# Optimization experiments

Measured on AMD Instinct MI355X. Metric: run time of the kernel, lower is better.

The kernel has to match this reference:

```python
import jax, jax.numpy as jnp
import numpy as np

# Dimensions (see init_kwargs): C=out_channels, R=res, PS=pool_size, HN=head_num,
# D=head_dim=R*R//HN, input spatial H=W=PS*R.
B, C, R, PS, HN, D = 16, 512, 32, 3, 8, 128
NORM_C = 0.5


def _avg_pool(x, k):
    b, c, h, w = x.shape
    return x.reshape(b, c, h // k, k, w // k, k).mean(axis=(3, 5))


def _max_pool(x, k):
    b, c, h, w = x.shape
    return x.reshape(b, c, h // k, k, w // k, k).max(axis=(3, 5))


def _to_heads(p):
    # Replicates torch: [B,C,R,R].view(B,R*R,C).permute(0,2,1).view(B,C,HN,D).permute(0,2,1,3)
    t = p.reshape(B, R * R, C).transpose(0, 2, 1)  # [B, C, R*R]
    return t.reshape(B, C, HN, D).transpose(0, 2, 1, 3)  # [B, HN, C, D]


def setup_inputs() -> dict:
    key = jax.random.key(0)
    ks = jax.random.split(key, 6)
    H = PS * R
    x = jax.random.normal(ks[0], (B, C, H, H), jnp.float32)
    # per-head q/k projections (Linear(head_dim, head_dim) per head)
    Wqk = jax.random.normal(ks[1], (HN, D, D), jnp.float32) * (1.0 / np.sqrt(D))
    bqk = jax.random.normal(ks[2], (HN, D), jnp.float32) * 0.01
    # w_p: Linear(C, C) feeding sigmoid gate
    Wp = jax.random.normal(ks[3], (C, C), jnp.float32) * (1.0 / np.sqrt(C))
    bp = jnp.zeros((C,), jnp.float32)
    # w_v: 1x1 Conv2d(C, C)
    Wv = jax.random.normal(ks[4], (C, C), jnp.float32) * (1.0 / np.sqrt(C))
    bv = jax.random.normal(ks[5], (C,), jnp.float32) * 0.01
    return {"x": x, "Wqk": Wqk, "bqk": bqk, "Wp": Wp, "bp": bp,
            "Wv": Wv, "bv": bv, "weight": 0}


def reference(x, Wqk, bqk, Wp, bp, Wv, bv, weight):
    # pooled query / key token grids: [B, C, R, R]
    q_pool = _avg_pool(x, PS)
    k_pool = _max_pool(x, PS)

    # heads over channels: [B, HN, C, D], then per-head linear (torch Linear: y = x W^T + b)
    q = jnp.einsum('bhcd,hed->bhce', _to_heads(q_pool), Wqk) + bqk[None, :, None, :]
    k = jnp.einsum('bhcd,hed->bhce', _to_heads(k_pool), Wqk) + bqk[None, :, None, :]

    # value: 1x1 conv then AvgPool2d(3) -> [B, HN, C, D]
    v_conv = jnp.einsum('bchw,oc->bohw', x, Wv) + bv[None, :, None, None]
    v = _to_heads(_avg_pool(v_conv, 3))

    # channel attention scores: [B, HN, C, C]
    scores = jnp.einsum('bhcd,bhed->bhce', q, k)
    # learned power-law exponent gate: sigmoid(Linear(mean over keys))
    p = jax.nn.sigmoid(scores.mean(axis=-1) @ Wp.T + bp)  # [B, HN, C]
    norm_scores = scores / jnp.power(jnp.float32(D), NORM_C + p[..., None])
    w = jax.nn.softmax(norm_scores, axis=-1)
    attn = jnp.einsum('bhce,bhed->bhcd', w, v)  # [B, HN, C, D]

    # back to [B, R, R, C] (torch permute/view chain)
    attn = attn.transpose(0, 2, 1, 3).reshape(B, C, R * R)
    attn = attn.transpose(0, 2, 1).reshape(B, R, R, C)

    # residual on pooled input (original code's residual shape is inconsistent;
    # we use the pooled token grid, same reshape path as the output)
    resid = q_pool.reshape(B, R * R, C).reshape(B, R, R, C)
    return resid + attn * (1 + weight)
```

## Files before the change

### kernel.cpp

```cpp
#include <hip/hip_runtime.h>
#include <math.h>

typedef unsigned short u16;
typedef short bf16x8 __attribute__((ext_vector_type(8)));
typedef float floatx4 __attribute__((ext_vector_type(4)));

#define F_QP   0ull
#define F_KP   8388608ull
#define F_KBAR 16777216ull
#define F_MROW 16793600ull
#define F_IPW  16859136ull
#define F_RS   16924672ull
#define F_END  16990208ull
#define U_QPT_V 0ull
#define U_QPT_P 8388608ull
#define U_KPT_P 16777216ull
#define U_PQ    25165824ull
#define U_PK    33554432ull
#define U_VP    41943040ull
#define U_E     50331648ull
#define U_WV    83886080ull
#define U_WQK   84148224ull

__device__ __forceinline__ u16 f2bf(float f) {
    union { float f; unsigned u; } v; v.f = f;
    return (u16)((v.u + 0x7fffu + ((v.u >> 16) & 1u)) >> 16);
}
__device__ __forceinline__ float bf2f(u16 u) {
    union { unsigned u; float f; } v; v.u = ((unsigned)u) << 16;
    return v.f;
}
__device__ __forceinline__ void ld_async16(const u16* g, u16* l) {
    __builtin_amdgcn_global_load_lds(
        (const __attribute__((address_space(1))) void*)g,
        (__attribute__((address_space(3))) void*)l, 16, 0, 0);
}

__global__ __launch_bounds__(256) void pool_kernel(const float* __restrict__ x,
                                                   float* __restrict__ qp,
                                                   float* __restrict__ kp) {
    int idx = blockIdx.x * 256 + threadIdx.x;
    int r = idx & 1023;
    int c = (idx >> 10) & 511;
    int b = idx >> 19;
    int i = r >> 5, j = r & 31;
    const float* p = x + b * 4718592 + c * 9216 + (3 * i) * 96 + 3 * j;
    float s = 0.f, mx = -INFINITY;
    #pragma unroll
    for (int di = 0; di < 3; ++di)
        #pragma unroll
        for (int dj = 0; dj < 3; ++dj) {
            float v = p[di * 96 + dj];
            s += v; mx = fmaxf(mx, v);
        }
    qp[idx] = s * (1.f / 9.f);
    kp[idx] = mx;
}

__global__ __launch_bounds__(256) void transpose_cvt(const float* __restrict__ in,
                                                     u16* __restrict__ out,
                                                     int inRows, int inCols) {
    __shared__ float tile[32][33];
    const float* src = in + (size_t)blockIdx.z * 524288;
    u16* dst = out + (size_t)blockIdx.z * 524288;
    int c0 = blockIdx.x * 32, r0 = blockIdx.y * 32;
    int tx = threadIdx.x & 31, ty = threadIdx.x >> 5;
    #pragma unroll
    for (int it = 0; it < 4; ++it)
        tile[ty + it * 8][tx] = src[(size_t)(r0 + ty + it * 8) * inCols + c0 + tx];
    __syncthreads();
    #pragma unroll
    for (int it = 0; it < 4; ++it)
        dst[(size_t)(c0 + ty + it * 8) * inRows + r0 + tx] = f2bf(tile[tx][ty + it * 8]);
}

__global__ __launch_bounds__(256) void cvt_bf16(const float* __restrict__ in,
                                                u16* __restrict__ out, int n) {
    int i = blockIdx.x * 256 + threadIdx.x;
    if (i < n) out[i] = f2bf(in[i]);
}

__global__ __launch_bounds__(256) void zero_f32(float* __restrict__ p, int n) {
    int i = blockIdx.x * 256 + threadIdx.x;
    if (i < n) p[i] = 0.f;
}

__device__ __forceinline__ void gemm_bt_body(const u16* __restrict__ A, int ldA,
                                             const u16* __restrict__ B, int ldB, int K,
                                             u16* As, u16* Bs, floatx4 (&acc)[4][4]) {
    const int tid = threadIdx.x;
    const int lane = tid & 63;
    const int wv = tid >> 6;
    const int wm = (wv & 1) * 64, wn = (wv >> 1) * 64;
    const u16* ga0 = A + (size_t)(tid >> 2) * ldA + (tid & 3) * 8;
    const u16* ga1 = A + (size_t)((tid >> 2) + 64) * ldA + (tid & 3) * 8;
    const u16* gb0 = B + (size_t)(tid >> 2) * ldB + (tid & 3) * 8;
    const u16* gb1 = B + (size_t)((tid >> 2) + 64) * ldB + (tid & 3) * 8;
    u16* la0 = As + tid * 8;
    u16* la1 = As + (tid + 256) * 8;
    u16* lb0 = Bs + tid * 8;
    u16* lb1 = Bs + (tid + 256) * 8;
    const int arow = (lane & 15) * 32 + (lane >> 4) * 8;
    for (int k0 = 0; k0 < K; k0 += 32) {
        ld_async16(ga0 + k0, la0);
        ld_async16(ga1 + k0, la1);
        ld_async16(gb0 + k0, lb0);
        ld_async16(gb1 + k0, lb1);
        __syncthreads();
        bf16x8 af[4], bfr[4];
        #pragma unroll
        for (int i = 0; i < 4; ++i)
            af[i] = *(const bf16x8*)&As[(wm + i * 16) * 32 + arow];
        #pragma unroll
        for (int j = 0; j < 4; ++j)
            bfr[j] = *(const bf16x8*)&Bs[(wn + j * 16) * 32 + arow];
        #pragma unroll
        for (int i = 0; i < 4; ++i)
            #pragma unroll
            for (int j = 0; j < 4; ++j)
                acc[i][j] = __builtin_amdgcn_mfma_f32_16x16x32_bf16(af[i], bfr[j], acc[i][j], 0, 0, 0);
        __syncthreads();
    }
}

__global__ __launch_bounds__(256) void vpool_mfma(const u16* __restrict__ Wv_bf,
                                                  const float* __restrict__ bv,
                                                  const u16* __restrict__ qpT_v,
                                                  u16* __restrict__ vp_bf) {
    __shared__ __align__(16) u16 As[4096], Bs[4096];
    floatx4 acc[4][4] = {};
    const int m0 = blockIdx.y * 128, n0 = blockIdx.x * 128, b = blockIdx.z;
    gemm_bt_body(Wv_bf + (size_t)m0 * 512, 512,
                 qpT_v + (size_t)b * 524288 + (size_t)n0 * 512, 512, 512, As, Bs, acc);
    const int tid = threadIdx.x, lane = tid & 63, wv = tid >> 6;
    const int wm = (wv & 1) * 64, wn = (wv >> 1) * 64, col = lane & 15, quad = lane >> 4;
    u16* outb = vp_bf + (size_t)b * 524288;
    #pragma unroll
    for (int i = 0; i < 4; ++i)
        #pragma unroll
        for (int r = 0; r < 4; ++r) {
            int m = m0 + wm + i * 16 + quad * 4 + r;
            float bias = bv[m];
            #pragma unroll
            for (int j = 0; j < 4; ++j) {
                int n = n0 + wn + j * 16 + col;
                outb[(size_t)m * 1024 + n] = f2bf(acc[i][j][r] + bias);
            }
        }
}

__global__ __launch_bounds__(256) void proj_mfma(const u16* __restrict__ qpT_p,
                                                 const u16* __restrict__ kpT_p,
                                                 const u16* __restrict__ Wqk_bf,
                                                 const float* __restrict__ bqk,
                                                 u16* __restrict__ pq_bf,
                                                 u16* __restrict__ pk_bf) {
    __shared__ __align__(16) u16 As[4096], Bs[4096];
    floatx4 acc[4][4] = {};
    const int z = blockIdx.y;
    const int b = z >> 4, h = (z >> 1) & 7, src = z & 1;
    const int m0 = blockIdx.x * 128;
    const u16* P = (src ? kpT_p : qpT_p) + (size_t)b * 524288 + (size_t)m0 * 1024 + h * 128;
    gemm_bt_body(P, 1024, Wqk_bf + h * 16384, 128, 128, As, Bs, acc);
    const int tid = threadIdx.x, lane = tid & 63, wv = tid >> 6;
    const int wm = (wv & 1) * 64, wn = (wv >> 1) * 64, col = lane & 15, quad = lane >> 4;
    u16* outp = (src ? pk_bf : pq_bf) + (size_t)(b * 8 + h) * 65536 + (size_t)m0 * 128;
    #pragma unroll
    for (int i = 0; i < 4; ++i)
        #pragma unroll
        for (int r = 0; r < 4; ++r) {
            int m = wm + i * 16 + quad * 4 + r;
            #pragma unroll
            for (int j = 0; j < 4; ++j) {
                int n = wn + j * 16 + col;
                outp[(size_t)m * 128 + n] = f2bf(acc[i][j][r] + bqk[h * 128 + n]);
            }
        }
}

__global__ __launch_bounds__(128) void kbar_kernel(const u16* __restrict__ pk_bf,
                                                   float* __restrict__ kbar) {
    int bh = blockIdx.x, d = threadIdx.x;
    const u16* p = pk_bf + (size_t)bh * 65536 + d;
    float s = 0.f;
    for (int e = 0; e < 512; ++e) s += bf2f(p[e * 128]);
    kbar[bh * 128 + d] = s * (1.f / 512.f);
}

__global__ __launch_bounds__(256) void mrow_kernel(const u16* __restrict__ pq_bf,
                                                   const float* __restrict__ kbar,
                                                   float* __restrict__ mrow) {
    __shared__ float kb[128];
    int bh = blockIdx.x, tid = threadIdx.x;
    if (tid < 128) kb[tid] = kbar[bh * 128 + tid];
    __syncthreads();
    for (int c = tid; c < 512; c += 256) {
        const u16* q = pq_bf + (size_t)bh * 65536 + c * 128;
        float s = 0.f;
        #pragma unroll 8
        for (int d = 0; d < 128; ++d) s += bf2f(q[d]) * kb[d];
        mrow[bh * 512 + c] = s;
    }
}

__global__ __launch_bounds__(256) void gate_kernel(const float* __restrict__ mrow,
                                                   const float* __restrict__ Wp,
                                                   const float* __restrict__ bp,
                                                   float* __restrict__ ipw) {
    __shared__ float ms[512];
    int bh = blockIdx.x, tid = threadIdx.x;
    for (int c = tid; c < 512; c += 256) ms[c] = mrow[bh * 512 + c];
    __syncthreads();
    for (int c2 = tid; c2 < 512; c2 += 256) {
        const float* wr = Wp + c2 * 512;
        float a = bp[c2];
        #pragma unroll 8
        for (int c = 0; c < 512; ++c) a += ms[c] * wr[c];
        float pg = 1.f / (1.f + expf(-a));
        ipw[bh * 512 + c2] = exp2f(-7.f * (0.5f + pg));
    }
}

__global__ __launch_bounds__(256) void scores_mfma(const u16* __restrict__ pq_bf,
                                                   const u16* __restrict__ pk_bf,
                                                   const float* __restrict__ ipw,
                                                   u16* __restrict__ e_bf,
                                                   float* __restrict__ rowsum) {
    __shared__ __align__(16) u16 As[4096], Bs[4096];
    floatx4 acc[4][4] = {};
    const int n0 = blockIdx.x * 128, m0 = blockIdx.y * 128, bh = blockIdx.z;
    gemm_bt_body(pq_bf + (size_t)bh * 65536 + (size_t)m0 * 128, 128,
                 pk_bf + (size_t)bh * 65536 + (size_t)n0 * 128, 128, 128, As, Bs, acc);
    const int tid = threadIdx.x, lane = tid & 63, wv = tid >> 6;
    const int wm = (wv & 1) * 64, wn = (wv >> 1) * 64, col = lane & 15, quad = lane >> 4;
    u16* ebase = e_bf + (size_t)bh * 262144;
    float* rs = rowsum + bh * 512;
    #pragma unroll
    for (int i = 0; i < 4; ++i)
        #pragma unroll
        for (int r = 0; r < 4; ++r) {
            int m = m0 + wm + i * 16 + quad * 4 + r;
            float sc = ipw[(size_t)bh * 512 + m];
            float p = 0.f;
            #pragma unroll
            for (int j = 0; j < 4; ++j) {
                int n = n0 + wn + j * 16 + col;
                u16 eb = f2bf(expf(acc[i][j][r] * sc));
                ebase[(size_t)m * 512 + n] = eb;
                p += bf2f(eb);
            }
            #pragma unroll
            for (int o = 8; o; o >>= 1) p += __shfl_xor(p, o);
            if (col == 0) atomicAdd(&rs[m], p);
        }
}

__global__ __launch_bounds__(256) void attn_out_mfma(const u16* __restrict__ vp_bf,
                                                     const u16* __restrict__ e_bf,
                                                     const float* __restrict__ rowsum,
                                                     const float* __restrict__ qp,
                                                     float* __restrict__ outp,
                                                     const int* __restrict__ wgt) {
    __shared__ __align__(16) u16 As[4096], Bs[4096];
    floatx4 acc[4][4] = {};
    const int n0 = blockIdx.x * 128, bh = blockIdx.y;
    const int b = bh >> 3, h = bh & 7;
    gemm_bt_body(vp_bf + (size_t)b * 524288 + (size_t)h * 65536, 512,
                 e_bf + (size_t)bh * 262144 + (size_t)n0 * 512, 512, 512, As, Bs, acc);
    const int tid = threadIdx.x, lane = tid & 63, wv = tid >> 6;
    const int wm = (wv & 1) * 64, wn = (wv >> 1) * 64, col = lane & 15, quad = lane >> 4;
    const float mult = 1.f + (float)wgt[0];
    #pragma unroll
    for (int j = 0; j < 4; ++j) {
        int n = n0 + wn + j * 16 + col;
        float inv = mult / rowsum[bh * 512 + n];
        #pragma unroll
        for (int i = 0; i < 4; ++i)
            #pragma unroll
            for (int r = 0; r < 4; ++r) {
                int m = wm + i * 16 + quad * 4 + r;
                size_t o = (size_t)b * 524288 + (size_t)(h * 128 + m) * 512 + n;
                outp[o] = qp[o] + acc[i][j][r] * inv;
            }
    }
}

extern "C" void kernel_launch(void* const* d_in, const int* in_sizes, int n_in,
                              void* d_out, int out_size, void* d_ws, size_t ws_size,
                              hipStream_t stream) {
    const float* x   = (const float*)d_in[0];
    const float* Wqk = (const float*)d_in[1];
    const float* bqk = (const float*)d_in[2];
    const float* Wp  = (const float*)d_in[3];
    const float* bp  = (const float*)d_in[4];
    const float* Wv  = (const float*)d_in[5];
    const float* bv  = (const float*)d_in[6];
    const int*   wgt = (const int*)d_in[7];
    float* out = (float*)d_out;

    float* ws = (float*)d_ws;
    float* qp   = ws + F_QP;
    float* kp   = ws + F_KP;
    float* kbar = ws + F_KBAR;
    float* mrow = ws + F_MROW;
    float* ipw  = ws + F_IPW;
    float* rs   = ws + F_RS;
    u16* ub = (u16*)(ws + F_END);
    u16* qpT_v  = ub + U_QPT_V;
    u16* qpT_p  = ub + U_QPT_P;
    u16* kpT_p  = ub + U_KPT_P;
    u16* pq_bf  = ub + U_PQ;
    u16* pk_bf  = ub + U_PK;
    u16* vp_bf  = ub + U_VP;
    u16* e_bf   = ub + U_E;
    u16* Wv_bf  = ub + U_WV;
    u16* Wqk_bf = ub + U_WQK;

    pool_kernel<<<32768, 256, 0, stream>>>(x, qp, kp);
    transpose_cvt<<<dim3(32, 16, 16), 256, 0, stream>>>(qp, qpT_v, 512, 1024);
    transpose_cvt<<<dim3(16, 32, 16), 256, 0, stream>>>(qp, qpT_p, 1024, 512);
    transpose_cvt<<<dim3(16, 32, 16), 256, 0, stream>>>(kp, kpT_p, 1024, 512);
    cvt_bf16<<<1024, 256, 0, stream>>>(Wv, Wv_bf, 262144);
    cvt_bf16<<<512, 256, 0, stream>>>(Wqk, Wqk_bf, 131072);
    zero_f32<<<256, 256, 0, stream>>>(rs, 65536);

    vpool_mfma<<<dim3(8, 4, 16), 256, 0, stream>>>(Wv_bf, bv, qpT_v, vp_bf);
    proj_mfma<<<dim3(4, 256), 256, 0, stream>>>(qpT_p, kpT_p, Wqk_bf, bqk, pq_bf, pk_bf);
    kbar_kernel<<<128, 128, 0, stream>>>(pk_bf, kbar);
    mrow_kernel<<<128, 256, 0, stream>>>(pq_bf, kbar, mrow);
    gate_kernel<<<128, 256, 0, stream>>>(mrow, Wp, bp, ipw);
    scores_mfma<<<dim3(4, 4, 128), 256, 0, stream>>>(pq_bf, pk_bf, ipw, e_bf, rs);
    attn_out_mfma<<<dim3(4, 128), 256, 0, stream>>>(vp_bf, e_bf, rs, qp, out, wgt);
}
```

Measured before the change: 632.9 us.

## Fuse pooling with transposes, fuse gate kernels, and flash-fuse scores with attention output

Pooling now writes the bf16 transposed layouts directly from a shared-memory tile, replacing three separate transpose passes and the kp buffer. The weight conversions are merged into one kernel, and Wp is pre-transposed so the gate GEMV reads it coalesced. The kbar, mrow and gate kernels become a single kernel. The scores and attention-output GEMMs are fused into one flash-style kernel that keeps the exp tile in LDS, which removes the 32M-element bf16 exp-score buffer and the global atomics for row sums. In exchange the fused kernel launches only 512 blocks, which may hurt occupancy and parallelism, and it uses fast exp without max subtraction.

Result: faster. 596.8 us (-5.7%).

```diff
diff --git a/kernel.cpp b/kernel.cpp
--- a/kernel.cpp
+++ b/kernel.cpp
@@ -6,21 +6,17 @@
 typedef float floatx4 __attribute__((ext_vector_type(4)));
 
 #define F_QP   0ull
-#define F_KP   8388608ull
-#define F_KBAR 16777216ull
-#define F_MROW 16793600ull
-#define F_IPW  16859136ull
-#define F_RS   16924672ull
-#define F_END  16990208ull
+#define F_IPW  8388608ull
+#define F_WPT  8454144ull
+#define F_END  8716288ull
 #define U_QPT_V 0ull
 #define U_QPT_P 8388608ull
 #define U_KPT_P 16777216ull
 #define U_PQ    25165824ull
 #define U_PK    33554432ull
 #define U_VP    41943040ull
-#define U_E     50331648ull
-#define U_WV    83886080ull
-#define U_WQK   84148224ull
+#define U_WV    50331648ull
+#define U_WQK   50593792ull
 
 __device__ __forceinline__ u16 f2bf(float f) {
     union { float f; unsigned u; } v; v.f = f;
@@ -36,53 +32,71 @@
         (__attribute__((address_space(3))) void*)l, 16, 0, 0);
 }
 
-__global__ __launch_bounds__(256) void pool_kernel(const float* __restrict__ x,
-                                                   float* __restrict__ qp,
-                                                   float* __restrict__ kp) {
-    int idx = blockIdx.x * 256 + threadIdx.x;
-    int r = idx & 1023;
-    int c = (idx >> 10) & 511;
-    int b = idx >> 19;
-    int i = r >> 5, j = r & 31;
-    const float* p = x + b * 4718592 + c * 9216 + (3 * i) * 96 + 3 * j;
-    float s = 0.f, mx = -INFINITY;
-    #pragma unroll
-    for (int di = 0; di < 3; ++di)
-        #pragma unroll
-        for (int dj = 0; dj < 3; ++dj) {
-            float v = p[di * 96 + dj];
-            s += v; mx = fmaxf(mx, v);
-        }
-    qp[idx] = s * (1.f / 9.f);
-    kp[idx] = mx;
-}
-
-__global__ __launch_bounds__(256) void transpose_cvt(const float* __restrict__ in,
-                                                     u16* __restrict__ out,
-                                                     int inRows, int inCols) {
-    __shared__ float tile[32][33];
-    const float* src = in + (size_t)blockIdx.z * 524288;
-    u16* dst = out + (size_t)blockIdx.z * 524288;
-    int c0 = blockIdx.x * 32, r0 = blockIdx.y * 32;
+__global__ __launch_bounds__(256) void pool_fused(const float* __restrict__ x,
+                                                  float* __restrict__ qp,
+                                                  u16* __restrict__ qpT_v,
+                                                  u16* __restrict__ qpT_p,
+                                                  u16* __restrict__ kpT_p) {
+    __shared__ float Tq[32][33], Tk[32][33];
+    const int tid = threadIdx.x;
+    const int i  = blockIdx.x;
+    const int c0 = blockIdx.y * 32;
+    const int b  = blockIdx.z;
+    const int j  = tid & 31, cg = tid >> 5;
+    #pragma unroll
+    for (int p = 0; p < 4; ++p) {
+        int cl = p * 8 + cg;
+        const float* px = x + (size_t)b * 4718592 + (size_t)(c0 + cl) * 9216 + (3 * i) * 96 + 3 * j;
+        float s = 0.f, mx = -INFINITY;
+        #pragma unroll
+        for (int di = 0; di < 3; ++di)
+            #pragma unroll
+            for (int dj = 0; dj < 3; ++dj) {
+                float v = px[di * 96 + dj];
+                s += v; mx = fmaxf(mx, v);
+            }
+        float q = s * (1.f / 9.f);
+        Tq[cl][j] = q; Tk[cl][j] = mx;
+        qp[(size_t)b * 524288 + (size_t)(c0 + cl) * 1024 + i * 32 + j] = q;
+    }
+    __syncthreads();
+    const int cl = tid & 31, jq = tid >> 5;
+    const int rh = i >> 4;
+    const int s2 = (c0 + cl) * 2 + rh;
+    #pragma unroll
+    for (int jj = 0; jj < 4; ++jj) {
+        int jw = jq + jj * 8;
+        int rr = i * 32 + jw;
+        int cc = rr & 511;
+        u16 qb = f2bf(Tq[cl][jw]);
+        u16 kb = f2bf(Tk[cl][jw]);
+        qpT_v[(size_t)b * 524288 + (size_t)rr * 512 + c0 + cl] = qb;
+        qpT_p[(size_t)b * 524288 + (size_t)cc * 1024 + s2] = qb;
+        kpT_p[(size_t)b * 524288 + (size_t)cc * 1024 + s2] = kb;
+    }
+}
+
+__global__ __launch_bounds__(256) void cvt_w(const float* __restrict__ Wv,
+                                             const float* __restrict__ Wqk,
+                                             u16* __restrict__ Wv_bf,
+                                             u16* __restrict__ Wqk_bf) {
+    int i = blockIdx.x * 256 + threadIdx.x;
+    if (i < 262144) Wv_bf[i] = f2bf(Wv[i]);
+    else if (i < 393216) Wqk_bf[i - 262144] = f2bf(Wqk[i - 262144]);
+}
+
+__global__ __launch_bounds__(256) void transpose_wp(const float* __restrict__ in,
+                                                    float* __restrict__ out) {
+    __shared__ float t[32][33];
+    int x0 = blockIdx.x * 32, y0 = blockIdx.y * 32;
     int tx = threadIdx.x & 31, ty = threadIdx.x >> 5;
     #pragma unroll
     for (int it = 0; it < 4; ++it)
-        tile[ty + it * 8][tx] = src[(size_t)(r0 + ty + it * 8) * inCols + c0 + tx];
+        t[ty + it * 8][tx] = in[(size_t)(y0 + ty + it * 8) * 512 + x0 + tx];
     __syncthreads();
     #pragma unroll
     for (int it = 0; it < 4; ++it)
-        dst[(size_t)(c0 + ty + it * 8) * inRows + r0 + tx] = f2bf(tile[tx][ty + it * 8]);
-}
-
-__global__ __launch_bounds__(256) void cvt_bf16(const float* __restrict__ in,
-                                                u16* __restrict__ out, int n) {
-    int i = blockIdx.x * 256 + threadIdx.x;
-    if (i < n) out[i] = f2bf(in[i]);
-}
-
-__global__ __launch_bounds__(256) void zero_f32(float* __restrict__ p, int n) {
-    int i = blockIdx.x * 256 + threadIdx.x;
-    if (i < n) p[i] = 0.f;
+        out[(size_t)(x0 + ty + it * 8) * 512 + y0 + tx] = t[tx][ty + it * 8];
 }
 
 __device__ __forceinline__ void gemm_bt_body(const u16* __restrict__ A, int ldA,
@@ -178,109 +192,139 @@
         }
 }
 
-__global__ __launch_bounds__(128) void kbar_kernel(const u16* __restrict__ pk_bf,
-                                                   float* __restrict__ kbar) {
-    int bh = blockIdx.x, d = threadIdx.x;
-    const u16* p = pk_bf + (size_t)bh * 65536 + d;
-    float s = 0.f;
-    for (int e = 0; e < 512; ++e) s += bf2f(p[e * 128]);
-    kbar[bh * 128 + d] = s * (1.f / 512.f);
-}
-
-__global__ __launch_bounds__(256) void mrow_kernel(const u16* __restrict__ pq_bf,
-                                                   const float* __restrict__ kbar,
-                                                   float* __restrict__ mrow) {
+__global__ __launch_bounds__(256) void gate_fused(const u16* __restrict__ pq_bf,
+                                                  const u16* __restrict__ pk_bf,
+                                                  const float* __restrict__ WpT,
+                                                  const float* __restrict__ bp,
+                                                  float* __restrict__ ipw) {
+    __shared__ float sp[256];
     __shared__ float kb[128];
-    int bh = blockIdx.x, tid = threadIdx.x;
-    if (tid < 128) kb[tid] = kbar[bh * 128 + tid];
-    __syncthreads();
-    for (int c = tid; c < 512; c += 256) {
-        const u16* q = pq_bf + (size_t)bh * 65536 + c * 128;
+    __shared__ float ms[512];
+    const int bh = blockIdx.x, tid = threadIdx.x;
+    const u16* pkb = pk_bf + (size_t)bh * 65536;
+    const u16* pqb = pq_bf + (size_t)bh * 65536;
+    {
+        int d = tid & 127, half = tid >> 7;
+        const u16* p = pkb + (size_t)(half * 256) * 128 + d;
+        float s = 0.f;
+        #pragma unroll 8
+        for (int e = 0; e < 256; ++e) s += bf2f(p[(size_t)e * 128]);
+        sp[tid] = s;
+    }
+    __syncthreads();
+    if (tid < 128) kb[tid] = (sp[tid] + sp[tid + 128]) * (1.f / 512.f);
+    __syncthreads();
+    for (int cc = tid; cc < 512; cc += 256) {
+        const u16* q = pqb + (size_t)cc * 128;
         float s = 0.f;
         #pragma unroll 8
         for (int d = 0; d < 128; ++d) s += bf2f(q[d]) * kb[d];
-        mrow[bh * 512 + c] = s;
-    }
-}
-
-__global__ __launch_bounds__(256) void gate_kernel(const float* __restrict__ mrow,
-                                                   const float* __restrict__ Wp,
-                                                   const float* __restrict__ bp,
-                                                   float* __restrict__ ipw) {
-    __shared__ float ms[512];
-    int bh = blockIdx.x, tid = threadIdx.x;
-    for (int c = tid; c < 512; c += 256) ms[c] = mrow[bh * 512 + c];
+        ms[cc] = s;
+    }
     __syncthreads();
     for (int c2 = tid; c2 < 512; c2 += 256) {
-        const float* wr = Wp + c2 * 512;
         float a = bp[c2];
-        #pragma unroll 8
-        for (int c = 0; c < 512; ++c) a += ms[c] * wr[c];
-        float pg = 1.f / (1.f + expf(-a));
+        #pragma unroll 4
+        for (int c = 0; c < 512; ++c) a += ms[c] * WpT[(size_t)c * 512 + c2];
+        float pg = 1.f / (1.f + __expf(-a));
         ipw[bh * 512 + c2] = exp2f(-7.f * (0.5f + pg));
     }
 }
 
-__global__ __launch_bounds__(256) void scores_mfma(const u16* __restrict__ pq_bf,
-                                                   const u16* __restrict__ pk_bf,
-                                                   const float* __restrict__ ipw,
-                                                   u16* __restrict__ e_bf,
-                                                   float* __restrict__ rowsum) {
-    __shared__ __align__(16) u16 As[4096], Bs[4096];
-    floatx4 acc[4][4] = {};
-    const int n0 = blockIdx.x * 128, m0 = blockIdx.y * 128, bh = blockIdx.z;
-    gemm_bt_body(pq_bf + (size_t)bh * 65536 + (size_t)m0 * 128, 128,
-                 pk_bf + (size_t)bh * 65536 + (size_t)n0 * 128, 128, 128, As, Bs, acc);
-    const int tid = threadIdx.x, lane = tid & 63, wv = tid >> 6;
-    const int wm = (wv & 1) * 64, wn = (wv >> 1) * 64, col = lane & 15, quad = lane >> 4;
-    u16* ebase = e_bf + (size_t)bh * 262144;
-    float* rs = rowsum + bh * 512;
-    #pragma unroll
-    for (int i = 0; i < 4; ++i)
-        #pragma unroll
-        for (int r = 0; r < 4; ++r) {
-            int m = m0 + wm + i * 16 + quad * 4 + r;
-            float sc = ipw[(size_t)bh * 512 + m];
-            float p = 0.f;
-            #pragma unroll
-            for (int j = 0; j < 4; ++j) {
-                int n = n0 + wn + j * 16 + col;
-                u16 eb = f2bf(expf(acc[i][j][r] * sc));
-                ebase[(size_t)m * 512 + n] = eb;
-                p += bf2f(eb);
-            }
-            #pragma unroll
-            for (int o = 8; o; o >>= 1) p += __shfl_xor(p, o);
-            if (col == 0) atomicAdd(&rs[m], p);
-        }
-}
-
-__global__ __launch_bounds__(256) void attn_out_mfma(const u16* __restrict__ vp_bf,
-                                                     const u16* __restrict__ e_bf,
-                                                     const float* __restrict__ rowsum,
+__global__ __launch_bounds__(256, 2) void flash_mfma(const u16* __restrict__ pq_bf,
+                                                     const u16* __restrict__ pk_bf,
+                                                     const u16* __restrict__ vp_bf,
+                                                     const float* __restrict__ ipw,
                                                      const float* __restrict__ qp,
                                                      float* __restrict__ outp,
                                                      const int* __restrict__ wgt) {
-    __shared__ __align__(16) u16 As[4096], Bs[4096];
-    floatx4 acc[4][4] = {};
-    const int n0 = blockIdx.x * 128, bh = blockIdx.y;
-    const int b = bh >> 3, h = bh & 7;
-    gemm_bt_body(vp_bf + (size_t)b * 524288 + (size_t)h * 65536, 512,
-                 e_bf + (size_t)bh * 262144 + (size_t)n0 * 512, 512, 512, As, Bs, acc);
+    __shared__ __align__(16) u16 As[4096];
+    __shared__ __align__(16) u16 Bs[4096];
+    __shared__ __align__(16) u16 Et[128 * 136];
+    __shared__ float rsS[128];
+    __shared__ float ipwS[128];
     const int tid = threadIdx.x, lane = tid & 63, wv = tid >> 6;
     const int wm = (wv & 1) * 64, wn = (wv >> 1) * 64, col = lane & 15, quad = lane >> 4;
+    const int bh = blockIdx.y, b = bh >> 3, h = bh & 7;
+    const int m0 = blockIdx.x * 128;
+    if (tid < 128) { rsS[tid] = 0.f; ipwS[tid] = ipw[bh * 512 + m0 + tid]; }
+    const u16* Aq = pq_bf + (size_t)bh * 65536 + (size_t)m0 * 128;
+    const u16* Bk = pk_bf + (size_t)bh * 65536;
+    const u16* Av = vp_bf + (size_t)b * 524288 + (size_t)h * 65536;
+    const int srow = tid >> 2, scol = (tid & 3) * 8;
+    u16 *la0 = As + tid * 8, *la1 = As + (tid + 256) * 8;
+    u16 *lb0 = Bs + tid * 8, *lb1 = Bs + (tid + 256) * 8;
+    const int arow = col * 32 + quad * 8;
+    floatx4 accP[4][4] = {};
+    __syncthreads();
+
+    for (int n0 = 0; n0 < 512; n0 += 128) {
+        floatx4 accS[4][4] = {};
+        for (int k0 = 0; k0 < 128; k0 += 32) {
+            ld_async16(Aq + (size_t)srow * 128 + k0 + scol, la0);
+            ld_async16(Aq + (size_t)(srow + 64) * 128 + k0 + scol, la1);
+            ld_async16(Bk + (size_t)(n0 + srow) * 128 + k0 + scol, lb0);
+            ld_async16(Bk + (size_t)(n0 + srow + 64) * 128 + k0 + scol, lb1);
+            __syncthreads();
+            bf16x8 af[4], bfr[4];
+            #pragma unroll
+            for (int i = 0; i < 4; ++i) af[i] = *(const bf16x8*)&As[(wm + i * 16) * 32 + arow];
+            #pragma unroll
+            for (int j = 0; j < 4; ++j) bfr[j] = *(const bf16x8*)&Bs[(wn + j * 16) * 32 + arow];
+            #pragma unroll
+            for (int i = 0; i < 4; ++i)
+                #pragma unroll
+                for (int j = 0; j < 4; ++j)
+                    accS[i][j] = __builtin_amdgcn_mfma_f32_16x16x32_bf16(af[i], bfr[j], accS[i][j], 0, 0, 0);
+            __syncthreads();
+        }
+        #pragma unroll
+        for (int i = 0; i < 4; ++i)
+            #pragma unroll
+            for (int r = 0; r < 4; ++r) {
+                int ml = wm + i * 16 + quad * 4 + r;
+                float sc = ipwS[ml];
+                float p = 0.f;
+                #pragma unroll
+                for (int j = 0; j < 4; ++j) {
+                    float e = __expf(accS[i][j][r] * sc);
+                    p += e;
+                    Et[ml * 136 + wn + j * 16 + col] = f2bf(e);
+                }
+                #pragma unroll
+                for (int o = 8; o; o >>= 1) p += __shfl_xor(p, o);
+                if (col == 0) atomicAdd(&rsS[ml], p);
+            }
+        __syncthreads();
+        for (int k0 = 0; k0 < 128; k0 += 32) {
+            ld_async16(Av + (size_t)srow * 512 + n0 + k0 + scol, la0);
+            ld_async16(Av + (size_t)(srow + 64) * 512 + n0 + k0 + scol, la1);
+            __syncthreads();
+            bf16x8 af[4], bfr[4];
+            #pragma unroll
+            for (int i = 0; i < 4; ++i) af[i] = *(const bf16x8*)&As[(wm + i * 16) * 32 + arow];
+            #pragma unroll
+            for (int j = 0; j < 4; ++j) bfr[j] = *(const bf16x8*)&Et[(wn + j * 16 + col) * 136 + k0 + quad * 8];
+            #pragma unroll
+            for (int i = 0; i < 4; ++i)
+                #pragma unroll
+                for (int j = 0; j < 4; ++j)
+                    accP[i][j] = __builtin_amdgcn_mfma_f32_16x16x32_bf16(af[i], bfr[j], accP[i][j], 0, 0, 0);
+            __syncthreads();
+        }
+    }
     const float mult = 1.f + (float)wgt[0];
     #pragma unroll
     for (int j = 0; j < 4; ++j) {
-        int n = n0 + wn + j * 16 + col;
-        float inv = mult / rowsum[bh * 512 + n];
+        int nl = wn + j * 16 + col;
+        float inv = mult / rsS[nl];
         #pragma unroll
         for (int i = 0; i < 4; ++i)
             #pragma unroll
             for (int r = 0; r < 4; ++r) {
-                int m = wm + i * 16 + quad * 4 + r;
-                size_t o = (size_t)b * 524288 + (size_t)(h * 128 + m) * 512 + n;
-                outp[o] = qp[o] + acc[i][j][r] * inv;
+                int d = wm + i * 16 + quad * 4 + r;
+                size_t o = (size_t)b * 524288 + (size_t)(h * 128 + d) * 512 + m0 + nl;
+                outp[o] = qp[o] + accP[i][j][r] * inv;
             }
     }
 }
@@ -299,12 +343,9 @@
     float* out = (float*)d_out;
 
     float* ws = (float*)d_ws;
-    float* qp   = ws + F_QP;
-    float* kp   = ws + F_KP;
-    float* kbar = ws + F_KBAR;
-    float* mrow = ws + F_MROW;
-    float* ipw  = ws + F_IPW;
-    float* rs   = ws + F_RS;
+    float* qp  = ws + F_QP;
+    float* ipw = ws + F_IPW;
+    float* WpT = ws + F_WPT;
     u16* ub = (u16*)(ws + F_END);
     u16* qpT_v  = ub + U_QPT_V;
     u16* qpT_p  = ub + U_QPT_P;
@@ -312,23 +353,14 @@
     u16* pq_bf  = ub + U_PQ;
     u16* pk_bf  = ub + U_PK;
     u16* vp_bf  = ub + U_VP;
-    u16* e_bf   = ub + U_E;
     u16* Wv_bf  = ub + U_WV;
     u16* Wqk_bf = ub + U_WQK;
 
-    pool_kernel<<<32768, 256, 0, stream>>>(x, qp, kp);
-    transpose_cvt<<<dim3(32, 16, 16), 256, 0, stream>>>(qp, qpT_v, 512, 1024);
-    transpose_cvt<<<dim3(16, 32, 16), 256, 0, stream>>>(qp, qpT_p, 1024, 512);
-    transpose_cvt<<<dim3(16, 32, 16), 256, 0, stream>>>(kp, kpT_p, 1024, 512);
-    cvt_bf16<<<1024, 256, 0, stream>>>(Wv, Wv_bf, 262144);
-    cvt_bf16<<<512, 256, 0, stream>>>(Wqk, Wqk_bf, 131072);
-    zero_f32<<<256, 256, 0, stream>>>(rs, 65536);
-
+    pool_fused<<<dim3(32, 16, 16), 256, 0, stream>>>(x, qp, qpT_v, qpT_p, kpT_p);
+    cvt_w<<<1536, 256, 0, stream>>>(Wv, Wqk, Wv_bf, Wqk_bf);
+    transpose_wp<<<dim3(16, 16), 256, 0, stream>>>(Wp, WpT);
     vpool_mfma<<<dim3(8, 4, 16), 256, 0, stream>>>(Wv_bf, bv, qpT_v, vp_bf);
     proj_mfma<<<dim3(4, 256), 256, 0, stream>>>(qpT_p, kpT_p, Wqk_bf, bqk, pq_bf, pk_bf);
-    kbar_kernel<<<128, 128, 0, stream>>>(pk_bf, kbar);
-    mrow_kernel<<<128, 256, 0, stream>>>(pq_bf, kbar, mrow);
-    gate_kernel<<<128, 256, 0, stream>>>(mrow, Wp, bp, ipw);
-    scores_mfma<<<dim3(4, 4, 128), 256, 0, stream>>>(pq_bf, pk_bf, ipw, e_bf, rs);
-    attn_out_mfma<<<dim3(4, 128), 256, 0, stream>>>(vp_bf, e_bf, rs, qp, out, wgt);
-}
+    gate_fused<<<128, 256, 0, stream>>>(pq_bf, pk_bf, WpT, bp, ipw);
+    flash_mfma<<<dim3(4, 128), 256, 0, stream>>>(pq_bf, pk_bf, vp_bf, ipw, qp, out, wgt);
+}
```
